# Kernel tuning notes

Hardware: AMD Instinct MI355X
Metric: run time of the kernel (lower is better)

Reference implementation:

```python
import jax, jax.numpy as jnp
import numpy as np

N = 1000; K = 500; M = N - K          # codeword / info / parity bits
NUE = 4; NBS = 4                      # tx / rx antennas
BPS = 4; RATE = 0.5; NSYM = N // BPS  # 16-QAM, 250 symbols per codeword
NITER = 5                             # BP iterations

# 16-QAM constellation, Gray-coded per axis (Sionna-style), unit energy
_bits = ((np.arange(16)[:, None] >> np.array([3, 2, 1, 0])) & 1).astype(np.float32)
_re = (1 - 2 * _bits[:, 0]) * (2 - (1 - 2 * _bits[:, 2]))
_im = (1 - 2 * _bits[:, 1]) * (2 - (1 - 2 * _bits[:, 3]))
POINTS = jnp.asarray((_re + 1j * _im) / np.sqrt(10.0), dtype=jnp.complex64)  # [16]
LABELS = jnp.asarray(_bits)  # [16,4] bit labels per point


def setup_inputs() -> dict:
    key = jax.random.key(0)
    ks = jax.random.split(key, 5)
    batch = 1000
    # systematic sparse LDPC-like code: H = [P^T | I_M], info-bit degree 3
    rs = np.random.RandomState(0)
    P = np.zeros((K, M), np.int32)
    for i in range(K):
        P[i, rs.choice(M, 3, replace=False)] = 1
    vi, ci = np.nonzero(P)
    vn = np.concatenate([vi, K + np.arange(M)]).astype(np.int32)  # [2000]
    cn = np.concatenate([ci, np.arange(M)]).astype(np.int32)      # [2000]
    b = jax.random.randint(ks[0], (batch, NUE, K), 0, 2, dtype=jnp.int32)
    h_re = jax.random.normal(ks[1], (batch * NSYM, NBS, NUE), jnp.float32)
    h_im = jax.random.normal(ks[2], (batch * NSYM, NBS, NUE), jnp.float32)
    n_re = jax.random.normal(ks[3], (batch * NSYM, NBS), jnp.float32)
    n_im = jax.random.normal(ks[4], (batch * NSYM, NBS), jnp.float32)
    return {"batch_size": batch, "ebno_db": jnp.full((1,), 5.0, jnp.float32),
            "b": b, "P": jnp.asarray(P), "cn_idx": jnp.asarray(cn),
            "vn_idx": jnp.asarray(vn), "h_re": h_re, "h_im": h_im,
            "noise_re": n_re, "noise_im": n_im}


def _forward(batch_size, ebno_db, b, P, cn_idx, vn_idx, h_re, h_im, noise_re, noise_im):
    no = 1.0 / (10.0 ** (ebno_db[0] / 10.0) * BPS * RATE)  # ebnodb2no
    # --- LDPC encode (systematic): c = [b, b@P mod 2] ---
    bf = b.astype(jnp.float32)
    parity = jnp.mod(jnp.round(bf @ P.astype(jnp.float32)), 2.0)
    c = jnp.concatenate([bf, parity], -1)                    # [B,NUE,N]
    # --- QAM mapper ---
    idx = (c.reshape(batch_size, NUE, NSYM, BPS) @ jnp.array([8., 4., 2., 1.], jnp.float32)).astype(jnp.int32)
    x = POINTS[idx]                                          # [B,NUE,NSYM]
    x_f = jnp.transpose(x, (0, 2, 1)).reshape(-1, NUE)       # [B*NSYM,NUE]
    # --- flat fading channel, h ~ CN(0,1), AWGN ---
    h = ((h_re + 1j * h_im) / np.sqrt(2.0)).astype(jnp.complex64)
    w = ((noise_re + 1j * noise_im) * jnp.sqrt(no / 2.0)).astype(jnp.complex64)
    y = jnp.einsum('bij,bj->bi', h, x_f) + w                 # [B*NSYM,NBS]
    # --- LMMSE equalizer: G = H^H (H H^H + no I)^-1, unbiased scaling ---
    A = jnp.einsum('bik,bjk->bij', h, jnp.conj(h)) \
        + no.astype(jnp.complex64) * jnp.eye(NBS, dtype=jnp.complex64)
    Ainv_y = jnp.linalg.solve(A, y[..., None])[..., 0]
    x_raw = jnp.einsum('bij,bi->bj', jnp.conj(h), Ainv_y)    # G y, [B*NSYM,NUE]
    GH = jnp.einsum('bij,bik->bjk', jnp.conj(h), jnp.linalg.solve(A, h))
    d = jnp.real(jnp.diagonal(GH, axis1=1, axis2=2))         # diag(GH), [B*NSYM,NUE]
    x_hat = x_raw / d.astype(jnp.complex64)
    no_eff = jnp.maximum(1.0 / d - 1.0, 1e-12)
    x_hat = jnp.transpose(x_hat.reshape(batch_size, NSYM, NUE), (0, 2, 1))  # [B,NUE,NSYM]
    nvar = jnp.transpose(no_eff.reshape(batch_size, NSYM, NUE), (0, 2, 1))
    # --- max-log demapper, L = log p(b=0)/p(b=1) ---
    metric = -(jnp.abs(x_hat[..., None] - POINTS) ** 2) / nvar[..., None]   # [B,NUE,NSYM,16]
    NEG = jnp.float32(-1e30)
    m5 = metric[..., None, :]                               # [B,NUE,NSYM,1,16]
    lab = LABELS.T[None, None, None]                        # [1,1,1,4,16]
    m0 = jnp.max(jnp.where(lab == 0, m5, NEG), -1)
    m1 = jnp.max(jnp.where(lab == 1, m5, NEG), -1)
    llr = (m0 - m1).reshape(batch_size, NUE, N)
    # --- LDPC BP decoder (sum-product over fixed sparse Tanner graph) ---
    Lch = llr.reshape(batch_size * NUE, N).T                # [N, Bc]
    c2v = jnp.zeros((cn_idx.shape[0], Lch.shape[1]), jnp.float32)  # [E, Bc]
    for _ in range(NITER):
        vtot = Lch.at[vn_idx].add(c2v)                      # Lch + segment_sum(c2v)
        m_vc = vtot[vn_idx] - c2v                           # extrinsic VN->CN
        t = jnp.tanh(jnp.clip(m_vc * 0.5, -9.9, 9.9))
        t = jnp.where(t >= 0, jnp.maximum(t, 1e-7), jnp.minimum(t, -1e-7))
        prod = jax.ops.segment_prod(t, cn_idx, num_segments=M)
        c2v = 2.0 * jnp.arctanh(jnp.clip(prod[cn_idx] / t, -0.999999, 0.999999))
    vtot = Lch.at[vn_idx].add(c2v)
    b_hat = (vtot[:K].T < 0).astype(jnp.float32).reshape(batch_size, NUE, K)
    return bf, b_hat


def reference(batch_size, ebno_db, b, P, cn_idx, vn_idx, h_re, h_im, noise_re, noise_im):
    return _forward(batch_size, ebno_db, b, P, cn_idx, vn_idx,
                    h_re, h_im, noise_re, noise_im)
```

## Files before the change

kernel.cpp:

```cpp
#include <hip/hip_runtime.h>
#include <math.h>

#define KK     500
#define MM     500
#define NNODES 1000
#define NSYM   250
#define NITERS 5
#define MAXVDEG 4
#define EMAX   2048
#define TB     256
#define LTB    64

__global__ void __launch_bounds__(512)
k_setup(const int* __restrict__ cn, const int* __restrict__ vn, int E,
        const float* __restrict__ ebno, const int* __restrict__ P,
        const int* __restrict__ b, int ncw,
        int* __restrict__ cinfo, int* __restrict__ vlist, int* __restrict__ coff,
        double* __restrict__ nobuf, unsigned* __restrict__ Ppack,
        unsigned* __restrict__ bpack, float* __restrict__ out, int packBlocks) {
  __shared__ int sdeg[512];
  __shared__ int ssc[512];
  __shared__ int scur[512];
  __shared__ int svc[NNODES];
  int tid = threadIdx.x;
  int bx = blockIdx.x;

  if (bx == 0) {
    sdeg[tid] = 0;
    for (int n = tid; n < NNODES; n += 512) svc[n] = 0;
    __syncthreads();
    for (int e = tid; e < E; e += 512) atomicAdd(&sdeg[cn[e]], 1);
    __syncthreads();
    int v = sdeg[tid];
    ssc[tid] = v;
    __syncthreads();
    for (int o = 1; o < 512; o <<= 1) {
      int x = (tid >= o) ? ssc[tid - o] : 0;
      __syncthreads();
      ssc[tid] += x;
      __syncthreads();
    }
    int excl = ssc[tid] - v;
    scur[tid] = excl;
    if (tid < MM) {
      coff[tid] = excl;
      if (tid == MM - 1) coff[MM] = ssc[tid];
    }
    __syncthreads();
    for (int e = tid; e < E; e += 512) {
      int c = cn[e], n = vn[e];
      int slot;
      if (n >= KK) {
        slot = ssc[c] - 1;
      } else {
        slot = atomicAdd(&scur[c], 1);
      }
      cinfo[slot] = (c << 16) | n;
      if (n < KK) {
        int t = atomicAdd(&svc[n], 1);
        if (t < MAXVDEG) vlist[n * MAXVDEG + t] = slot;
      }
    }
    if (tid == 0) {
      double no = 1.0 / (pow(10.0, (double)ebno[0] * 0.1) * 2.0);
      nobuf[0] = no;
      nobuf[1] = sqrt(no * 0.5);
    }
    return;
  }

  if (bx <= packBlocks) {
    int id = (bx - 1) * 512 + tid;
    if (id < MM * 16) {
      int j = id >> 4, w = id & 15;
      unsigned word = 0u;
      int base = w * 32;
      for (int bit = 0; bit < 32; ++bit) {
        int i = base + bit;
        if (i < KK && P[i * MM + j] != 0) word |= (1u << bit);
      }
      Ppack[j * 16 + w] = word;
    } else {
      int id2 = id - MM * 16;
      if (id2 < ncw * 16) {
        int cw = id2 >> 4, w = id2 & 15;
        unsigned word = 0u;
        int base = w * 32;
        for (int bit = 0; bit < 32; ++bit) {
          int i = base + bit;
          if (i < KK && b[cw * KK + i] != 0) word |= (1u << bit);
        }
        bpack[cw * 16 + w] = word;
      }
    }
    return;
  }

  int id = (bx - 1 - packBlocks) * 512 + tid;
  if (id < ncw * KK) out[id] = (float)b[id];
}

__device__ __forceinline__ void qam_pointf(int p, float& re, float& im) {
  const float s = 0.31622776601683794f;
  int b0 = (p >> 3) & 1, b1 = (p >> 2) & 1, b2 = (p >> 1) & 1, b3 = p & 1;
  re = (float)((1 - 2 * b0) * (2 - (1 - 2 * b2))) * s;
  im = (float)((1 - 2 * b1) * (2 - (1 - 2 * b3))) * s;
}

__global__ void __launch_bounds__(LTB, 1)
k_lmmse(const float* __restrict__ h_re, const float* __restrict__ h_im,
        const float* __restrict__ n_re, const float* __restrict__ n_im,
        const double* __restrict__ nobuf,
        const unsigned* __restrict__ bpack, const unsigned* __restrict__ Ppack,
        float* __restrict__ Lch3, int T, int ncw) {
  int t = blockIdx.x * blockDim.x + threadIdx.x;
  if (t >= T) return;
  int bt = t / NSYM, s = t - bt * NSYM;

  float no = (float)nobuf[0];
  float sq = (float)nobuf[1];
  const float is2 = 0.70710678118654752f;

  float Hr[4][4], Hi[4][4];
  {
    const float4* hr4 = (const float4*)h_re;
    const float4* hi4 = (const float4*)h_im;
    #pragma unroll
    for (int i = 0; i < 4; ++i) {
      float4 a = hr4[t * 4 + i], c = hi4[t * 4 + i];
      Hr[i][0] = a.x * is2; Hr[i][1] = a.y * is2;
      Hr[i][2] = a.z * is2; Hr[i][3] = a.w * is2;
      Hi[i][0] = c.x * is2; Hi[i][1] = c.y * is2;
      Hi[i][2] = c.z * is2; Hi[i][3] = c.w * is2;
    }
  }

  float xr[4], xi[4];
  #pragma unroll
  for (int ue = 0; ue < 4; ++ue) {
    const unsigned* bp = bpack + (bt * 4 + ue) * 16;
    int v = 0;
    #pragma unroll
    for (int k = 0; k < 4; ++k) {
      int n = 4 * s + k;
      int bit;
      if (n < KK) {
        bit = (bp[n >> 5] >> (n & 31)) & 1;
      } else {
        const unsigned* pp = Ppack + (n - KK) * 16;
        int cnt = 0;
        #pragma unroll
        for (int w = 0; w < 16; ++w) cnt += __popc(bp[w] & pp[w]);
        bit = cnt & 1;
      }
      v = (v << 1) | bit;
    }
    qam_pointf(v, xr[ue], xi[ue]);
  }

  float yr[4], yi[4];
  {
    float4 wr = ((const float4*)n_re)[t];
    float4 wi = ((const float4*)n_im)[t];
    float wrv[4] = {wr.x, wr.y, wr.z, wr.w};
    float wiv[4] = {wi.x, wi.y, wi.z, wi.w};
    #pragma unroll
    for (int i = 0; i < 4; ++i) {
      float ar = wrv[i] * sq;
      float ai = wiv[i] * sq;
      #pragma unroll
      for (int j = 0; j < 4; ++j) {
        ar += Hr[i][j] * xr[j] - Hi[i][j] * xi[j];
        ai += Hr[i][j] * xi[j] + Hi[i][j] * xr[j];
      }
      yr[i] = ar; yi[i] = ai;
    }
  }

  auto dotc = [&](int i, int j, float& ar, float& ai) {
    float r = 0.0f, m = 0.0f;
    #pragma unroll
    for (int k = 0; k < 4; ++k) {
      r += Hr[i][k] * Hr[j][k] + Hi[i][k] * Hi[j][k];
      m += Hi[i][k] * Hr[j][k] - Hr[i][k] * Hi[j][k];
    }
    ar = r; ai = m;
  };
  float a00, a11, a22, a33, dum;
  float a10r, a10i, a20r, a20i, a21r, a21i, a30r, a30i, a31r, a31i, a32r, a32i;
  dotc(0, 0, a00, dum);  a00 += no;
  dotc(1, 0, a10r, a10i);
  dotc(1, 1, a11, dum);  a11 += no;
  dotc(2, 0, a20r, a20i);
  dotc(2, 1, a21r, a21i);
  dotc(2, 2, a22, dum);  a22 += no;
  dotc(3, 0, a30r, a30i);
  dotc(3, 1, a31r, a31i);
  dotc(3, 2, a32r, a32i);
  dotc(3, 3, a33, dum);  a33 += no;

  float i00 = rsqrtf(a00);
  float L10r = a10r * i00, L10i = a10i * i00;
  float L20r = a20r * i00, L20i = a20i * i00;
  float L30r = a30r * i00, L30i = a30i * i00;
  float d11 = a11 - (L10r * L10r + L10i * L10i);
  float i11 = rsqrtf(d11);
  float L21r = (a21r - (L20r * L10r + L20i * L10i)) * i11;
  float L21i = (a21i - (L20i * L10r - L20r * L10i)) * i11;
  float L31r = (a31r - (L30r * L10r + L30i * L10i)) * i11;
  float L31i = (a31i - (L30i * L10r - L30r * L10i)) * i11;
  float d22 = a22 - (L20r * L20r + L20i * L20i) - (L21r * L21r + L21i * L21i);
  float i22 = rsqrtf(d22);
  float L32r = (a32r - (L30r * L20r + L30i * L20i) - (L31r * L21r + L31i * L21i)) * i22;
  float L32i = (a32i - (L30i * L20r - L30r * L20i) - (L31i * L21r - L31r * L21i)) * i22;
  float d33 = a33 - (L30r * L30r + L30i * L30i) - (L31r * L31r + L31i * L31i)
                  - (L32r * L32r + L32i * L32i);
  float i33 = rsqrtf(d33);

  #pragma unroll
  for (int j = 0; j < 4; ++j) {
    float u0r = Hr[0][j] * i00,               u0i = Hi[0][j] * i00;
    float u1r = (Hr[1][j] - (L10r * u0r - L10i * u0i)) * i11;
    float u1i = (Hi[1][j] - (L10r * u0i + L10i * u0r)) * i11;
    float u2r = (Hr[2][j] - (L20r * u0r - L20i * u0i) - (L21r * u1r - L21i * u1i)) * i22;
    float u2i = (Hi[2][j] - (L20r * u0i + L20i * u0r) - (L21r * u1i + L21i * u1r)) * i22;
    float u3r = (Hr[3][j] - (L30r * u0r - L30i * u0i) - (L31r * u1r - L31i * u1i)
                          - (L32r * u2r - L32i * u2i)) * i33;
    float u3i = (Hi[3][j] - (L30r * u0i + L30i * u0r) - (L31r * u1i + L31i * u1r)
                          - (L32r * u2i + L32i * u2r)) * i33;
    Hr[0][j] = u0r; Hi[0][j] = u0i; Hr[1][j] = u1r; Hi[1][j] = u1i;
    Hr[2][j] = u2r; Hi[2][j] = u2i; Hr[3][j] = u3r; Hi[3][j] = u3i;
  }
  {
    float v0r = yr[0] * i00,               v0i = yi[0] * i00;
    float v1r = (yr[1] - (L10r * v0r - L10i * v0i)) * i11;
    float v1i = (yi[1] - (L10r * v0i + L10i * v0r)) * i11;
    float v2r = (yr[2] - (L20r * v0r - L20i * v0i) - (L21r * v1r - L21i * v1i)) * i22;
    float v2i = (yi[2] - (L20r * v0i + L20i * v0r) - (L21r * v1i + L21i * v1r)) * i22;
    float v3r = (yr[3] - (L30r * v0r - L30i * v0i) - (L31r * v1r - L31i * v1i)
                       - (L32r * v2r - L32i * v2i)) * i33;
    float v3i = (yi[3] - (L30r * v0i + L30i * v0r) - (L31r * v1i + L31i * v1r)
                       - (L32r * v2i + L32i * v2r)) * i33;
    yr[0] = v0r; yi[0] = v0i; yr[1] = v1r; yi[1] = v1i;
    yr[2] = v2r; yi[2] = v2i; yr[3] = v3r; yi[3] = v3i;
  }

  const float PRT[16] = { 0.31622776601683794f, 0.31622776601683794f, 0.9486832980505138f, 0.9486832980505138f,
                          0.31622776601683794f, 0.31622776601683794f, 0.9486832980505138f, 0.9486832980505138f,
                         -0.31622776601683794f,-0.31622776601683794f,-0.9486832980505138f,-0.9486832980505138f,
                         -0.31622776601683794f,-0.31622776601683794f,-0.9486832980505138f,-0.9486832980505138f };
  const float PIT[16] = { 0.31622776601683794f, 0.9486832980505138f, 0.31622776601683794f, 0.9486832980505138f,
                         -0.31622776601683794f,-0.9486832980505138f,-0.31622776601683794f,-0.9486832980505138f,
                          0.31622776601683794f, 0.9486832980505138f, 0.31622776601683794f, 0.9486832980505138f,
                         -0.31622776601683794f,-0.9486832980505138f,-0.31622776601683794f,-0.9486832980505138f };

  float llr[4][4];
  #pragma unroll
  for (int j = 0; j < 4; ++j) {
    float dj = 0.0f, rr = 0.0f, ri = 0.0f;
    #pragma unroll
    for (int i = 0; i < 4; ++i) {
      dj += Hr[i][j] * Hr[i][j] + Hi[i][j] * Hi[i][j];
      rr += Hr[i][j] * yr[i] + Hi[i][j] * yi[i];
      ri += Hr[i][j] * yi[i] - Hi[i][j] * yr[i];
    }
    float rdj = __fdividef(1.0f, dj);
    float xhr = rr * rdj, xhi = ri * rdj;
    float gap = 1.0f - dj;
    float inoe = __fdividef(dj, fmaxf(gap, dj * 1e-12f));

    float m0[4] = {-1e30f, -1e30f, -1e30f, -1e30f};
    float m1[4] = {-1e30f, -1e30f, -1e30f, -1e30f};
    #pragma unroll
    for (int p = 0; p < 16; ++p) {
      float dr = xhr - PRT[p], di = xhi - PIT[p];
      float met = -(dr * dr + di * di) * inoe;
      #pragma unroll
      for (int k = 0; k < 4; ++k) {
        if ((p >> (3 - k)) & 1) m1[k] = fmaxf(m1[k], met);
        else                    m0[k] = fmaxf(m0[k], met);
      }
    }
    #pragma unroll
    for (int k = 0; k < 4; ++k) llr[k][j] = m0[k] - m1[k];
  }

  float2* pl0 = (float2*)(Lch3 + (size_t)bt * (NNODES * 4));
  float2* pl1 = pl0 + NNODES;
  #pragma unroll
  for (int k = 0; k < 4; ++k) {
    int node = 4 * s + k;
    pl0[node] = make_float2(llr[k][0], llr[k][1]);
    pl1[node] = make_float2(llr[k][2], llr[k][3]);
  }
}

__device__ __forceinline__ float tanh_half(float m) {
  float mc = fminf(fmaxf(m, -19.8f), 19.8f);
  float e = __expf(mc);
  float t = 1.0f - __fdividef(2.0f, e + 1.0f);
  return (t >= 0.0f) ? fmaxf(t, 1e-7f) : fminf(t, -1e-7f);
}
__device__ __forceinline__ float pclip(float P, float t) {
  return copysignf(fminf(fabsf(P), 0.999999f * fabsf(t)), P);
}
__device__ __forceinline__ float tfloor(float t) {
  return (t >= 0.0f) ? fmaxf(t, 1e-7f) : fminf(t, -1e-7f);
}
__device__ __forceinline__ float atanh2c(float P, float t) {
  float r = __fdividef(P, t);
  r = fminf(fmaxf(r, -0.999999f), 0.999999f);
  return __logf(__fdividef(1.0f + r, 1.0f - r));
}

__global__ void __launch_bounds__(256) k_bp(const float* __restrict__ Lch3,
                                            const int* __restrict__ vlist,
                                            const int* __restrict__ coff,
                                            const int* __restrict__ cinfo,
                                            float* __restrict__ out, int E, int ncw) {
  __shared__ float2 sT[EMAX];
  __shared__ float2 sP[512];

  int tid = threadIdx.x;
  int pairId = blockIdx.x;

  const float2* src = (const float2*)(Lch3 + (size_t)pairId * (NNODES * 2));

  float2 Ln[2], En[2];
  int pk0[2], pk1[2], pk2[2]; bool iok[2];
  #pragma unroll
  for (int i = 0; i < 2; ++i) {
    int n = tid + TB * i;
    iok[i] = n < KK;
    Ln[i] = make_float2(0.f, 0.f);
    En[i] = make_float2(1.f, 1.f);
    pk0[i] = pk1[i] = pk2[i] = 0;
    if (iok[i]) {
      float2 L = src[n];
      Ln[i] = L;
      En[i] = make_float2(__expf(fminf(fmaxf(L.x, -55.f), 55.f)),
                          __expf(fminf(fmaxf(L.y, -55.f), 55.f)));
      int s0 = vlist[n * MAXVDEG], s1 = vlist[n * MAXVDEG + 1], s2 = vlist[n * MAXVDEG + 2];
      pk0[i] = (cinfo[s0] & 0xffff0000) | s0;
      pk1[i] = (cinfo[s1] & 0xffff0000) | s1;
      pk2[i] = (cinfo[s2] & 0xffff0000) | s2;
    }
  }
  float2 qpar0, qpar1;
  {
    float2 Lp0 = src[KK + tid];
    qpar0 = make_float2(tanh_half(Lp0.x), tanh_half(Lp0.y));
  }
  bool c1ok = (tid + TB) < MM;
  if (c1ok) {
    float2 Lp1 = src[KK + tid + TB];
    qpar1 = make_float2(tanh_half(Lp1.x), tanh_half(Lp1.y));
  } else {
    qpar1 = make_float2(1.f, 1.f);
  }
  int beg0 = coff[tid], end0 = coff[tid + 1];
  int beg1 = c1ok ? coff[tid + TB] : 0;
  int end1 = c1ok ? coff[tid + TB + 1] : 0;

  for (int it = 0; it < NITERS; ++it) {
    if (it == 0) {
      #pragma unroll
      for (int i = 0; i < 2; ++i) {
        if (iok[i]) {
          float2 t = make_float2(tanh_half(Ln[i].x), tanh_half(Ln[i].y));
          sT[pk0[i] & 0xffff] = t;
          sT[pk1[i] & 0xffff] = t;
          sT[pk2[i] & 0xffff] = t;
        }
      }
    } else {
      #pragma unroll
      for (int i = 0; i < 2; ++i) {
        if (iok[i]) {
          int s0 = pk0[i] & 0xffff, c0 = ((unsigned)pk0[i]) >> 16;
          int s1 = pk1[i] & 0xffff, c1 = ((unsigned)pk1[i]) >> 16;
          int s2 = pk2[i] & 0xffff, c2 = ((unsigned)pk2[i]) >> 16;
          float2 P0 = sP[c0], P1 = sP[c1], P2 = sP[c2];
          float2 t0 = sT[s0], t1 = sT[s1], t2 = sT[s2];
          float p0 = pclip(P0.x, t0.x), p1 = pclip(P1.x, t1.x), p2 = pclip(P2.x, t2.x);
          float a0 = t0.x + p0, a1 = t1.x + p1, a2 = t2.x + p2;
          float b0 = t0.x - p0, b1 = t1.x - p1, b2 = t2.x - p2;
          float Ex = En[i].x;
          float A0 = Ex * (a1 * a2), A1 = Ex * (a0 * a2), A2 = Ex * (a0 * a1);
          float B0 = b1 * b2,        B1 = b0 * b2,        B2 = b0 * b1;
          float n0x = tfloor(__fdividef(A0 - B0, A0 + B0));
          float n1x = tfloor(__fdividef(A1 - B1, A1 + B1));
          float n2x = tfloor(__fdividef(A2 - B2, A2 + B2));
          float q0 = pclip(P0.y, t0.y), q1 = pclip(P1.y, t1.y), q2 = pclip(P2.y, t2.y);
          float c0a = t0.y + q0, c1a = t1.y + q1, c2a = t2.y + q2;
          float d0b = t0.y - q0, d1b = t1.y - q1, d2b = t2.y - q2;
          float Ey = En[i].y;
          float C0 = Ey * (c1a * c2a), C1 = Ey * (c0a * c2a), C2 = Ey * (c0a * c1a);
          float D0 = d1b * d2b,        D1 = d0b * d2b,        D2 = d0b * d1b;
          float n0y = tfloor(__fdividef(C0 - D0, C0 + D0));
          float n1y = tfloor(__fdividef(C1 - D1, C1 + D1));
          float n2y = tfloor(__fdividef(C2 - D2, C2 + D2));
          sT[s0] = make_float2(n0x, n0y);
          sT[s1] = make_float2(n1x, n1y);
          sT[s2] = make_float2(n2x, n2y);
        }
      }
    }
    __syncthreads();
    {
      float px = qpar0.x, py = qpar0.y;
      for (int e = beg0; e < end0 - 1; ++e) { float2 tt = sT[e]; px *= tt.x; py *= tt.y; }
      sP[tid] = make_float2(px, py);
      if (c1ok) {
        float qx = qpar1.x, qy = qpar1.y;
        for (int e = beg1; e < end1 - 1; ++e) { float2 tt = sT[e]; qx *= tt.x; qy *= tt.y; }
        sP[tid + TB] = make_float2(qx, qy);
      }
    }
    __syncthreads();
  }

  int cw0 = pairId * 2;
  float* o0 = out + (size_t)ncw * KK + (size_t)cw0 * KK;
  float* o1 = o0 + KK;
  #pragma unroll
  for (int i = 0; i < 2; ++i) {
    if (iok[i]) {
      int n = tid + TB * i;
      int s0 = pk0[i] & 0xffff, c0 = ((unsigned)pk0[i]) >> 16;
      int s1 = pk1[i] & 0xffff, c1 = ((unsigned)pk1[i]) >> 16;
      int s2 = pk2[i] & 0xffff, c2 = ((unsigned)pk2[i]) >> 16;
      float2 P0 = sP[c0], P1 = sP[c1], P2 = sP[c2];
      float2 t0 = sT[s0], t1 = sT[s1], t2 = sT[s2];
      float2 L = Ln[i];
      float ax = L.x + atanh2c(P0.x, t0.x) + atanh2c(P1.x, t1.x) + atanh2c(P2.x, t2.x);
      float ay = L.y + atanh2c(P0.y, t0.y) + atanh2c(P1.y, t1.y) + atanh2c(P2.y, t2.y);
      o0[n] = (ax < 0.0f) ? 1.0f : 0.0f;
      o1[n] = (ay < 0.0f) ? 1.0f : 0.0f;
    }
  }
}

extern "C" void kernel_launch(void* const* d_in, const int* in_sizes, int n_in,
                              void* d_out, int out_size, void* d_ws, size_t ws_size,
                              hipStream_t stream) {
  const float* ebno = (const float*)d_in[1];
  const int*   b    = (const int*)d_in[2];
  const int*   P    = (const int*)d_in[3];
  const int*   cn   = (const int*)d_in[4];
  const int*   vn   = (const int*)d_in[5];
  const float* h_re = (const float*)d_in[6];
  const float* h_im = (const float*)d_in[7];
  const float* nre  = (const float*)d_in[8];
  const float* nim  = (const float*)d_in[9];
  float* out = (float*)d_out;

  int E     = in_sizes[4];
  int batch = in_sizes[2] / (4 * KK);
  int ncw   = batch * 4;
  int T     = batch * NSYM;

  char* ws = (char*)d_ws;
  size_t off = 0;
  auto alloc = [&](size_t bytes) -> void* {
    void* p = ws + off;
    off += (bytes + 255) & ~(size_t)255;
    return p;
  };
  float*    Lch3   = (float*)alloc((size_t)NNODES * ncw * 4);
  unsigned* Ppack  = (unsigned*)alloc((size_t)MM * 16 * 4);
  unsigned* bpack  = (unsigned*)alloc((size_t)ncw * 16 * 4);
  int*      coff   = (int*)alloc((size_t)(MM + 1) * 4);
  int*      cinfo  = (int*)alloc((size_t)EMAX * 4);
  int*      vlist  = (int*)alloc((size_t)NNODES * MAXVDEG * 4);
  double*   nobuf  = (double*)alloc(2 * 8);
  (void)ws_size; (void)n_in; (void)out_size;

  int packItems  = MM * 16 + ncw * 16;
  int packBlocks = (packItems + 511) / 512;
  int bfBlocks   = (ncw * KK + 511) / 512;
  int setupGrid  = 1 + packBlocks + bfBlocks;

  k_setup<<<dim3(setupGrid), dim3(512), 0, stream>>>(cn, vn, E, ebno, P, b, ncw,
                                                     cinfo, vlist, coff, nobuf,
                                                     Ppack, bpack, out, packBlocks);
  k_lmmse<<<dim3((T + LTB - 1) / LTB), dim3(LTB), 0, stream>>>(h_re, h_im, nre, nim, nobuf,
                                                               bpack, Ppack, Lch3, T, ncw);
  k_bp<<<dim3(ncw / 2), dim3(TB), 0, stream>>>(Lch3, vlist, coff, cinfo, out, E, ncw);
}
```

Measured before the change: 180.0 us.

## Fuse LMMSE equalization and demapping into the BP decoder kernel via shared memory

```diff
diff --git a/kernel.cpp b/kernel.cpp
--- a/kernel.cpp
+++ b/kernel.cpp
@@ -9,7 +9,6 @@
 #define MAXVDEG 4
 #define EMAX   2048
 #define TB     256
-#define LTB    64
 
 __global__ void __launch_bounds__(512)
 k_setup(const int* __restrict__ cn, const int* __restrict__ vn, int E,
@@ -107,194 +106,6 @@
   im = (float)((1 - 2 * b1) * (2 - (1 - 2 * b3))) * s;
 }
 
-__global__ void __launch_bounds__(LTB, 1)
-k_lmmse(const float* __restrict__ h_re, const float* __restrict__ h_im,
-        const float* __restrict__ n_re, const float* __restrict__ n_im,
-        const double* __restrict__ nobuf,
-        const unsigned* __restrict__ bpack, const unsigned* __restrict__ Ppack,
-        float* __restrict__ Lch3, int T, int ncw) {
-  int t = blockIdx.x * blockDim.x + threadIdx.x;
-  if (t >= T) return;
-  int bt = t / NSYM, s = t - bt * NSYM;
-
-  float no = (float)nobuf[0];
-  float sq = (float)nobuf[1];
-  const float is2 = 0.70710678118654752f;
-
-  float Hr[4][4], Hi[4][4];
-  {
-    const float4* hr4 = (const float4*)h_re;
-    const float4* hi4 = (const float4*)h_im;
-    #pragma unroll
-    for (int i = 0; i < 4; ++i) {
-      float4 a = hr4[t * 4 + i], c = hi4[t * 4 + i];
-      Hr[i][0] = a.x * is2; Hr[i][1] = a.y * is2;
-      Hr[i][2] = a.z * is2; Hr[i][3] = a.w * is2;
-      Hi[i][0] = c.x * is2; Hi[i][1] = c.y * is2;
-      Hi[i][2] = c.z * is2; Hi[i][3] = c.w * is2;
-    }
-  }
-
-  float xr[4], xi[4];
-  #pragma unroll
-  for (int ue = 0; ue < 4; ++ue) {
-    const unsigned* bp = bpack + (bt * 4 + ue) * 16;
-    int v = 0;
-    #pragma unroll
-    for (int k = 0; k < 4; ++k) {
-      int n = 4 * s + k;
-      int bit;
-      if (n < KK) {
-        bit = (bp[n >> 5] >> (n & 31)) & 1;
-      } else {
-        const unsigned* pp = Ppack + (n - KK) * 16;
-        int cnt = 0;
-        #pragma unroll
-        for (int w = 0; w < 16; ++w) cnt += __popc(bp[w] & pp[w]);
-        bit = cnt & 1;
-      }
-      v = (v << 1) | bit;
-    }
-    qam_pointf(v, xr[ue], xi[ue]);
-  }
-
-  float yr[4], yi[4];
-  {
-    float4 wr = ((const float4*)n_re)[t];
-    float4 wi = ((const float4*)n_im)[t];
-    float wrv[4] = {wr.x, wr.y, wr.z, wr.w};
-    float wiv[4] = {wi.x, wi.y, wi.z, wi.w};
-    #pragma unroll
-    for (int i = 0; i < 4; ++i) {
-      float ar = wrv[i] * sq;
-      float ai = wiv[i] * sq;
-      #pragma unroll
-      for (int j = 0; j < 4; ++j) {
-        ar += Hr[i][j] * xr[j] - Hi[i][j] * xi[j];
-        ai += Hr[i][j] * xi[j] + Hi[i][j] * xr[j];
-      }
-      yr[i] = ar; yi[i] = ai;
-    }
-  }
-
-  auto dotc = [&](int i, int j, float& ar, float& ai) {
-    float r = 0.0f, m = 0.0f;
-    #pragma unroll
-    for (int k = 0; k < 4; ++k) {
-      r += Hr[i][k] * Hr[j][k] + Hi[i][k] * Hi[j][k];
-      m += Hi[i][k] * Hr[j][k] - Hr[i][k] * Hi[j][k];
-    }
-    ar = r; ai = m;
-  };
-  float a00, a11, a22, a33, dum;
-  float a10r, a10i, a20r, a20i, a21r, a21i, a30r, a30i, a31r, a31i, a32r, a32i;
-  dotc(0, 0, a00, dum);  a00 += no;
-  dotc(1, 0, a10r, a10i);
-  dotc(1, 1, a11, dum);  a11 += no;
-  dotc(2, 0, a20r, a20i);
-  dotc(2, 1, a21r, a21i);
-  dotc(2, 2, a22, dum);  a22 += no;
-  dotc(3, 0, a30r, a30i);
-  dotc(3, 1, a31r, a31i);
-  dotc(3, 2, a32r, a32i);
-  dotc(3, 3, a33, dum);  a33 += no;
-
-  float i00 = rsqrtf(a00);
-  float L10r = a10r * i00, L10i = a10i * i00;
-  float L20r = a20r * i00, L20i = a20i * i00;
-  float L30r = a30r * i00, L30i = a30i * i00;
-  float d11 = a11 - (L10r * L10r + L10i * L10i);
-  float i11 = rsqrtf(d11);
-  float L21r = (a21r - (L20r * L10r + L20i * L10i)) * i11;
-  float L21i = (a21i - (L20i * L10r - L20r * L10i)) * i11;
-  float L31r = (a31r - (L30r * L10r + L30i * L10i)) * i11;
-  float L31i = (a31i - (L30i * L10r - L30r * L10i)) * i11;
-  float d22 = a22 - (L20r * L20r + L20i * L20i) - (L21r * L21r + L21i * L21i);
-  float i22 = rsqrtf(d22);
-  float L32r = (a32r - (L30r * L20r + L30i * L20i) - (L31r * L21r + L31i * L21i)) * i22;
-  float L32i = (a32i - (L30i * L20r - L30r * L20i) - (L31i * L21r - L31r * L21i)) * i22;
-  float d33 = a33 - (L30r * L30r + L30i * L30i) - (L31r * L31r + L31i * L31i)
-                  - (L32r * L32r + L32i * L32i);
-  float i33 = rsqrtf(d33);
-
-  #pragma unroll
-  for (int j = 0; j < 4; ++j) {
-    float u0r = Hr[0][j] * i00,               u0i = Hi[0][j] * i00;
-    float u1r = (Hr[1][j] - (L10r * u0r - L10i * u0i)) * i11;
-    float u1i = (Hi[1][j] - (L10r * u0i + L10i * u0r)) * i11;
-    float u2r = (Hr[2][j] - (L20r * u0r - L20i * u0i) - (L21r * u1r - L21i * u1i)) * i22;
-    float u2i = (Hi[2][j] - (L20r * u0i + L20i * u0r) - (L21r * u1i + L21i * u1r)) * i22;
-    float u3r = (Hr[3][j] - (L30r * u0r - L30i * u0i) - (L31r * u1r - L31i * u1i)
-                          - (L32r * u2r - L32i * u2i)) * i33;
-    float u3i = (Hi[3][j] - (L30r * u0i + L30i * u0r) - (L31r * u1i + L31i * u1r)
-                          - (L32r * u2i + L32i * u2r)) * i33;
-    Hr[0][j] = u0r; Hi[0][j] = u0i; Hr[1][j] = u1r; Hi[1][j] = u1i;
-    Hr[2][j] = u2r; Hi[2][j] = u2i; Hr[3][j] = u3r; Hi[3][j] = u3i;
-  }
-  {
-    float v0r = yr[0] * i00,               v0i = yi[0] * i00;
-    float v1r = (yr[1] - (L10r * v0r - L10i * v0i)) * i11;
-    float v1i = (yi[1] - (L10r * v0i + L10i * v0r)) * i11;
-    float v2r = (yr[2] - (L20r * v0r - L20i * v0i) - (L21r * v1r - L21i * v1i)) * i22;
-    float v2i = (yi[2] - (L20r * v0i + L20i * v0r) - (L21r * v1i + L21i * v1r)) * i22;
-    float v3r = (yr[3] - (L30r * v0r - L30i * v0i) - (L31r * v1r - L31i * v1i)
-                       - (L32r * v2r - L32i * v2i)) * i33;
-    float v3i = (yi[3] - (L30r * v0i + L30i * v0r) - (L31r * v1i + L31i * v1r)
-                       - (L32r * v2i + L32i * v2r)) * i33;
-    yr[0] = v0r; yi[0] = v0i; yr[1] = v1r; yi[1] = v1i;
-    yr[2] = v2r; yi[2] = v2i; yr[3] = v3r; yi[3] = v3i;
-  }
-
-  const float PRT[16] = { 0.31622776601683794f, 0.31622776601683794f, 0.9486832980505138f, 0.9486832980505138f,
-                          0.31622776601683794f, 0.31622776601683794f, 0.9486832980505138f, 0.9486832980505138f,
-                         -0.31622776601683794f,-0.31622776601683794f,-0.9486832980505138f,-0.9486832980505138f,
-                         -0.31622776601683794f,-0.31622776601683794f,-0.9486832980505138f,-0.9486832980505138f };
-  const float PIT[16] = { 0.31622776601683794f, 0.9486832980505138f, 0.31622776601683794f, 0.9486832980505138f,
-                         -0.31622776601683794f,-0.9486832980505138f,-0.31622776601683794f,-0.9486832980505138f,
-                          0.31622776601683794f, 0.9486832980505138f, 0.31622776601683794f, 0.9486832980505138f,
-                         -0.31622776601683794f,-0.9486832980505138f,-0.31622776601683794f,-0.9486832980505138f };
-
-  float llr[4][4];
-  #pragma unroll
-  for (int j = 0; j < 4; ++j) {
-    float dj = 0.0f, rr = 0.0f, ri = 0.0f;
-    #pragma unroll
-    for (int i = 0; i < 4; ++i) {
-      dj += Hr[i][j] * Hr[i][j] + Hi[i][j] * Hi[i][j];
-      rr += Hr[i][j] * yr[i] + Hi[i][j] * yi[i];
-      ri += Hr[i][j] * yi[i] - Hi[i][j] * yr[i];
-    }
-    float rdj = __fdividef(1.0f, dj);
-    float xhr = rr * rdj, xhi = ri * rdj;
-    float gap = 1.0f - dj;
-    float inoe = __fdividef(dj, fmaxf(gap, dj * 1e-12f));
-
-    float m0[4] = {-1e30f, -1e30f, -1e30f, -1e30f};
-    float m1[4] = {-1e30f, -1e30f, -1e30f, -1e30f};
-    #pragma unroll
-    for (int p = 0; p < 16; ++p) {
-      float dr = xhr - PRT[p], di = xhi - PIT[p];
-      float met = -(dr * dr + di * di) * inoe;
-      #pragma unroll
-      for (int k = 0; k < 4; ++k) {
-        if ((p >> (3 - k)) & 1) m1[k] = fmaxf(m1[k], met);
-        else                    m0[k] = fmaxf(m0[k], met);
-      }
-    }
-    #pragma unroll
-    for (int k = 0; k < 4; ++k) llr[k][j] = m0[k] - m1[k];
-  }
-
-  float2* pl0 = (float2*)(Lch3 + (size_t)bt * (NNODES * 4));
-  float2* pl1 = pl0 + NNODES;
-  #pragma unroll
-  for (int k = 0; k < 4; ++k) {
-    int node = 4 * s + k;
-    pl0[node] = make_float2(llr[k][0], llr[k][1]);
-    pl1[node] = make_float2(llr[k][2], llr[k][3]);
-  }
-}
-
 __device__ __forceinline__ float tanh_half(float m) {
   float mc = fminf(fmaxf(m, -19.8f), 19.8f);
   float e = __expf(mc);
@@ -313,18 +124,198 @@
   return __logf(__fdividef(1.0f + r, 1.0f - r));
 }
 
-__global__ void __launch_bounds__(256) k_bp(const float* __restrict__ Lch3,
-                                            const int* __restrict__ vlist,
-                                            const int* __restrict__ coff,
-                                            const int* __restrict__ cinfo,
-                                            float* __restrict__ out, int E, int ncw) {
+#define SOLVE_DEMAP(J, Lout) {                                                          \
+  float u0r = Hr[0][J] * i00,               u0i = Hi[0][J] * i00;                       \
+  float u1r = (Hr[1][J] - (L10r * u0r - L10i * u0i)) * i11;                             \
+  float u1i = (Hi[1][J] - (L10r * u0i + L10i * u0r)) * i11;                             \
+  float u2r = (Hr[2][J] - (L20r * u0r - L20i * u0i) - (L21r * u1r - L21i * u1i)) * i22; \
+  float u2i = (Hi[2][J] - (L20r * u0i + L20i * u0r) - (L21r * u1i + L21i * u1r)) * i22; \
+  float u3r = (Hr[3][J] - (L30r * u0r - L30i * u0i) - (L31r * u1r - L31i * u1i)         \
+                        - (L32r * u2r - L32i * u2i)) * i33;                             \
+  float u3i = (Hi[3][J] - (L30r * u0i + L30i * u0r) - (L31r * u1i + L31i * u1r)         \
+                        - (L32r * u2i + L32i * u2r)) * i33;                             \
+  float dj = (u0r * u0r + u0i * u0i) + (u1r * u1r + u1i * u1i)                          \
+           + (u2r * u2r + u2i * u2i) + (u3r * u3r + u3i * u3i);                         \
+  float rr = (u0r * yr[0] + u0i * yi[0]) + (u1r * yr[1] + u1i * yi[1])                  \
+           + (u2r * yr[2] + u2i * yi[2]) + (u3r * yr[3] + u3i * yi[3]);                 \
+  float ri = (u0r * yi[0] - u0i * yr[0]) + (u1r * yi[1] - u1i * yr[1])                  \
+           + (u2r * yi[2] - u2i * yr[2]) + (u3r * yi[3] - u3i * yr[3]);                 \
+  float rdj = __fdividef(1.0f, dj);                                                    \
+  float xhr = rr * rdj, xhi = ri * rdj;                                                \
+  float gap = 1.0f - dj;                                                               \
+  float inoe = __fdividef(dj, fmaxf(gap, dj * 1e-12f));                                \
+  float m0[4] = {-1e30f, -1e30f, -1e30f, -1e30f};                                      \
+  float m1[4] = {-1e30f, -1e30f, -1e30f, -1e30f};                                      \
+  _Pragma("unroll")                                                                    \
+  for (int p = 0; p < 16; ++p) {                                                       \
+    float dr = xhr - PRT[p], di = xhi - PIT[p];                                        \
+    float met = -(dr * dr + di * di) * inoe;                                           \
+    _Pragma("unroll")                                                                  \
+    for (int k = 0; k < 4; ++k) {                                                      \
+      if ((p >> (3 - k)) & 1) m1[k] = fmaxf(m1[k], met);                               \
+      else                    m0[k] = fmaxf(m0[k], met);                               \
+    }                                                                                  \
+  }                                                                                    \
+  _Pragma("unroll")                                                                    \
+  for (int k = 0; k < 4; ++k) Lout[k] = m0[k] - m1[k];                                 \
+}
+
+__global__ void __launch_bounds__(256, 4)
+k_fused(const float* __restrict__ h_re, const float* __restrict__ h_im,
+        const float* __restrict__ n_re, const float* __restrict__ n_im,
+        const double* __restrict__ nobuf,
+        const unsigned* __restrict__ bpack, const unsigned* __restrict__ Ppack,
+        const int* __restrict__ vlist, const int* __restrict__ coff,
+        const int* __restrict__ cinfo, float* __restrict__ out, int ncw) {
   __shared__ float2 sT[EMAX];
   __shared__ float2 sP[512];
+  __shared__ float2 sL[NNODES];
 
   int tid = threadIdx.x;
   int pairId = blockIdx.x;
-
-  const float2* src = (const float2*)(Lch3 + (size_t)pairId * (NNODES * 2));
+  int bt = pairId >> 1, plane = pairId & 1;
+
+  if (tid < NSYM) {
+    int t = bt * NSYM + tid;
+    int s = tid;
+
+    float no = (float)nobuf[0];
+    float sq = (float)nobuf[1];
+    const float is2 = 0.70710678118654752f;
+
+    float Hr[4][4], Hi[4][4];
+    {
+      const float4* hr4 = (const float4*)h_re;
+      const float4* hi4 = (const float4*)h_im;
+      #pragma unroll
+      for (int i = 0; i < 4; ++i) {
+        float4 a = hr4[t * 4 + i], c = hi4[t * 4 + i];
+        Hr[i][0] = a.x * is2; Hr[i][1] = a.y * is2;
+        Hr[i][2] = a.z * is2; Hr[i][3] = a.w * is2;
+        Hi[i][0] = c.x * is2; Hi[i][1] = c.y * is2;
+        Hi[i][2] = c.z * is2; Hi[i][3] = c.w * is2;
+      }
+    }
+
+    float xr[4], xi[4];
+    #pragma unroll
+    for (int ue = 0; ue < 4; ++ue) {
+      const unsigned* bp = bpack + (bt * 4 + ue) * 16;
+      int v = 0;
+      #pragma unroll
+      for (int k = 0; k < 4; ++k) {
+        int n = 4 * s + k;
+        int bit;
+        if (n < KK) {
+          bit = (bp[n >> 5] >> (n & 31)) & 1;
+        } else {
+          const unsigned* pp = Ppack + (n - KK) * 16;
+          int cnt = 0;
+          #pragma unroll
+          for (int w = 0; w < 16; ++w) cnt += __popc(bp[w] & pp[w]);
+          bit = cnt & 1;
+        }
+        v = (v << 1) | bit;
+      }
+      qam_pointf(v, xr[ue], xi[ue]);
+    }
+
+    float yr[4], yi[4];
+    {
+      float4 wr = ((const float4*)n_re)[t];
+      float4 wi = ((const float4*)n_im)[t];
+      float wrv[4] = {wr.x, wr.y, wr.z, wr.w};
+      float wiv[4] = {wi.x, wi.y, wi.z, wi.w};
+      #pragma unroll
+      for (int i = 0; i < 4; ++i) {
+        float ar = wrv[i] * sq;
+        float ai = wiv[i] * sq;
+        #pragma unroll
+        for (int j = 0; j < 4; ++j) {
+          ar += Hr[i][j] * xr[j] - Hi[i][j] * xi[j];
+          ai += Hr[i][j] * xi[j] + Hi[i][j] * xr[j];
+        }
+        yr[i] = ar; yi[i] = ai;
+      }
+    }
+
+    auto dotc = [&](int i, int j, float& ar, float& ai) {
+      float r = 0.0f, m = 0.0f;
+      #pragma unroll
+      for (int k = 0; k < 4; ++k) {
+        r += Hr[i][k] * Hr[j][k] + Hi[i][k] * Hi[j][k];
+        m += Hi[i][k] * Hr[j][k] - Hr[i][k] * Hi[j][k];
+      }
+      ar = r; ai = m;
+    };
+    float a00, a11, a22, a33, dum;
+    float a10r, a10i, a20r, a20i, a21r, a21i, a30r, a30i, a31r, a31i, a32r, a32i;
+    dotc(0, 0, a00, dum);  a00 += no;
+    dotc(1, 0, a10r, a10i);
+    dotc(1, 1, a11, dum);  a11 += no;
+    dotc(2, 0, a20r, a20i);
+    dotc(2, 1, a21r, a21i);
+    dotc(2, 2, a22, dum);  a22 += no;
+    dotc(3, 0, a30r, a30i);
+    dotc(3, 1, a31r, a31i);
+    dotc(3, 2, a32r, a32i);
+    dotc(3, 3, a33, dum);  a33 += no;
+
+    float i00 = rsqrtf(a00);
+    float L10r = a10r * i00, L10i = a10i * i00;
+    float L20r = a20r * i00, L20i = a20i * i00;
+    float L30r = a30r * i00, L30i = a30i * i00;
+    float d11 = a11 - (L10r * L10r + L10i * L10i);
+    float i11 = rsqrtf(d11);
+    float L21r = (a21r - (L20r * L10r + L20i * L10i)) * i11;
+    float L21i = (a21i - (L20i * L10r - L20r * L10i)) * i11;
+    float L31r = (a31r - (L30r * L10r + L30i * L10i)) * i11;
+    float L31i = (a31i - (L30i * L10r - L30r * L10i)) * i11;
+    float d22 = a22 - (L20r * L20r + L20i * L20i) - (L21r * L21r + L21i * L21i);
+    float i22 = rsqrtf(d22);
+    float L32r = (a32r - (L30r * L20r + L30i * L20i) - (L31r * L21r + L31i * L21i)) * i22;
+    float L32i = (a32i - (L30i * L20r - L30r * L20i) - (L31i * L21r - L31r * L21i)) * i22;
+    float d33 = a33 - (L30r * L30r + L30i * L30i) - (L31r * L31r + L31i * L31i)
+                    - (L32r * L32r + L32i * L32i);
+    float i33 = rsqrtf(d33);
+
+    {
+      float v0r = yr[0] * i00,               v0i = yi[0] * i00;
+      float v1r = (yr[1] - (L10r * v0r - L10i * v0i)) * i11;
+      float v1i = (yi[1] - (L10r * v0i + L10i * v0r)) * i11;
+      float v2r = (yr[2] - (L20r * v0r - L20i * v0i) - (L21r * v1r - L21i * v1i)) * i22;
+      float v2i = (yi[2] - (L20r * v0i + L20i * v0r) - (L21r * v1i + L21i * v1r)) * i22;
+      float v3r = (yr[3] - (L30r * v0r - L30i * v0i) - (L31r * v1r - L31i * v1i)
+                         - (L32r * v2r - L32i * v2i)) * i33;
+      float v3i = (yi[3] - (L30r * v0i + L30i * v0r) - (L31r * v1i + L31i * v1r)
+                         - (L32r * v2i + L32i * v2r)) * i33;
+      yr[0] = v0r; yi[0] = v0i; yr[1] = v1r; yi[1] = v1i;
+      yr[2] = v2r; yi[2] = v2i; yr[3] = v3r; yi[3] = v3i;
+    }
+
+    const float PRT[16] = { 0.31622776601683794f, 0.31622776601683794f, 0.9486832980505138f, 0.9486832980505138f,
+                            0.31622776601683794f, 0.31622776601683794f, 0.9486832980505138f, 0.9486832980505138f,
+                           -0.31622776601683794f,-0.31622776601683794f,-0.9486832980505138f,-0.9486832980505138f,
+                           -0.31622776601683794f,-0.31622776601683794f,-0.9486832980505138f,-0.9486832980505138f };
+    const float PIT[16] = { 0.31622776601683794f, 0.9486832980505138f, 0.31622776601683794f, 0.9486832980505138f,
+                           -0.31622776601683794f,-0.9486832980505138f,-0.31622776601683794f,-0.9486832980505138f,
+                            0.31622776601683794f, 0.9486832980505138f, 0.31622776601683794f, 0.9486832980505138f,
+                           -0.31622776601683794f,-0.9486832980505138f,-0.31622776601683794f,-0.9486832980505138f };
+
+    float lA[4], lB[4];
+    if (plane == 0) {
+      SOLVE_DEMAP(0, lA);
+      SOLVE_DEMAP(1, lB);
+    } else {
+      SOLVE_DEMAP(2, lA);
+      SOLVE_DEMAP(3, lB);
+    }
+    #pragma unroll
+    for (int k = 0; k < 4; ++k) {
+      sL[4 * s + k] = make_float2(lA[k], lB[k]);
+    }
+  }
+  __syncthreads();
 
   float2 Ln[2], En[2];
   int pk0[2], pk1[2], pk2[2]; bool iok[2];
@@ -336,7 +327,7 @@
     En[i] = make_float2(1.f, 1.f);
     pk0[i] = pk1[i] = pk2[i] = 0;
     if (iok[i]) {
-      float2 L = src[n];
+      float2 L = sL[n];
       Ln[i] = L;
       En[i] = make_float2(__expf(fminf(fmaxf(L.x, -55.f), 55.f)),
                           __expf(fminf(fmaxf(L.y, -55.f), 55.f)));
@@ -348,12 +339,12 @@
   }
   float2 qpar0, qpar1;
   {
-    float2 Lp0 = src[KK + tid];
+    float2 Lp0 = sL[KK + tid];
     qpar0 = make_float2(tanh_half(Lp0.x), tanh_half(Lp0.y));
   }
   bool c1ok = (tid + TB) < MM;
   if (c1ok) {
-    float2 Lp1 = src[KK + tid + TB];
+    float2 Lp1 = sL[KK + tid + TB];
     qpar1 = make_float2(tanh_half(Lp1.x), tanh_half(Lp1.y));
   } else {
     qpar1 = make_float2(1.f, 1.f);
@@ -458,7 +449,6 @@
   int E     = in_sizes[4];
   int batch = in_sizes[2] / (4 * KK);
   int ncw   = batch * 4;
-  int T     = batch * NSYM;
 
   char* ws = (char*)d_ws;
   size_t off = 0;
@@ -467,7 +457,6 @@
     off += (bytes + 255) & ~(size_t)255;
     return p;
   };
-  float*    Lch3   = (float*)alloc((size_t)NNODES * ncw * 4);
   unsigned* Ppack  = (unsigned*)alloc((size_t)MM * 16 * 4);
   unsigned* bpack  = (unsigned*)alloc((size_t)ncw * 16 * 4);
   int*      coff   = (int*)alloc((size_t)(MM + 1) * 4);
@@ -484,7 +473,7 @@
   k_setup<<<dim3(setupGrid), dim3(512), 0, stream>>>(cn, vn, E, ebno, P, b, ncw,
                                                      cinfo, vlist, coff, nobuf,
                                                      Ppack, bpack, out, packBlocks);
-  k_lmmse<<<dim3((T + LTB - 1) / LTB), dim3(LTB), 0, stream>>>(h_re, h_im, nre, nim, nobuf,
-                                                               bpack, Ppack, Lch3, T, ncw);
-  k_bp<<<dim3(ncw / 2), dim3(TB), 0, stream>>>(Lch3, vlist, coff, cinfo, out, E, ncw);
-}
+  k_fused<<<dim3(ncw / 2), dim3(256), 0, stream>>>(h_re, h_im, nre, nim, nobuf,
+                                                   bpack, Ppack, vlist, coff, cinfo,
+                                                   out, ncw);
+}
```

Result: no change. 178.6 us (-0.8%).
